# Kernel tuning notes

Measured on AMD Instinct MI355X. Metric: run time of the kernel, lower is better.

## Reference

```python
import jax, jax.numpy as jnp
import numpy as np

NBITS = 3      # weight LSQ bits
PBITS = 8      # partial-sum LSQ bits
EPS = 1e-5


def round_ste(x):
    # straight-through round: identity gradient
    return x + jax.lax.stop_gradient(jnp.round(x) - x)


def lsq(x, alpha, nbits):
    # learned-step-size quantize/dequantize (symmetric signed)
    qn = -(2 ** (nbits - 1))
    qp = 2 ** (nbits - 1) - 1
    return round_ste(jnp.clip(x / alpha, qn, qp)) * alpha


def split_views(x):
    # x: [B,C,H,W] -> 9 shifted views of the 1-padded input, stacked [9,B,C,H,W]
    B, C, H, W = x.shape
    xp = jnp.pad(x, ((0, 0), (0, 0), (1, 1), (1, 1)))
    views = [xp[:, :, di:di + H, dj:dj + W] for dj in range(3) for di in range(3)]
    return jnp.stack(views, 0)


def split_conv3x3(x, w, wa, pa):
    # 3x3 conv emulated as 9 shifted 1x1 LSQ convs with quantized partial-sum accumulate
    # w: [9,O,C] per-tap 1x1 weights, wa: [9] weight step sizes, pa: [9] psum step sizes
    xs = split_views(x)                                      # [9,B,C,H,W]
    wq = jax.vmap(lambda wk, ak: lsq(wk, ak, NBITS))(w, wa)  # [9,O,C]
    ps = jnp.einsum('kbchw,koc->kbohw', xs, wq)              # 9 partial sums
    psq = lsq(ps, pa[:, None, None, None, None], PBITS)      # PartialSumLSQ each tap
    return psq.sum(0)                                        # accumulate -> [B,O,H,W]


def batchnorm(x, g, b):
    m = x.mean((0, 2, 3), keepdims=True)
    v = x.var((0, 2, 3), keepdims=True)
    return (x - m) / jnp.sqrt(v + EPS) * g[None, :, None, None] + b[None, :, None, None]


def setup_inputs() -> dict:
    key = jax.random.key(0)
    ks = jax.random.split(key, 8)
    B, C, O, H, W = 16, 128, 128, 56, 56
    x = jax.random.normal(ks[0], (B, C, H, W), jnp.float32)
    w1 = jax.random.normal(ks[1], (9, O, C), jnp.float32) * 0.05
    w2 = jax.random.normal(ks[2], (9, O, O), jnp.float32) * 0.05
    qp_w = 2 ** (NBITS - 1) - 1
    wa1 = 2.0 * jnp.mean(jnp.abs(w1), axis=(1, 2)) / np.sqrt(qp_w)
    wa2 = 2.0 * jnp.mean(jnp.abs(w2), axis=(1, 2)) / np.sqrt(qp_w)
    pa1 = jnp.full((9,), 0.05, jnp.float32)
    pa2 = jnp.full((9,), 0.05, jnp.float32)
    g1 = jnp.ones((O,), jnp.float32); b1 = jnp.zeros((O,), jnp.float32)
    g2 = jnp.ones((O,), jnp.float32); b2 = jnp.zeros((O,), jnp.float32)
    return {'x': x, 'w1': w1, 'wa1': wa1, 'pa1': pa1, 'g1': g1, 'b1': b1,
            'w2': w2, 'wa2': wa2, 'pa2': pa2, 'g2': g2, 'b2': b2}


def reference(x, w1, wa1, pa1, g1, b1, w2, wa2, pa2, g2, b2):
    identity = x
    out = split_conv3x3(x, w1, wa1, pa1)
    out = jax.nn.relu(batchnorm(out, g1, b1))
    out = split_conv3x3(out, w2, wa2, pa2)
    out = batchnorm(out, g2, b2)
    return jax.nn.relu(out + identity)
```

## Files before the change

### kernel.cpp

```cpp
#include <hip/hip_runtime.h>
#include <math.h>

typedef _Float16 f16;
typedef _Float16 half8 __attribute__((ext_vector_type(8)));
typedef float floatx16 __attribute__((ext_vector_type(16)));
typedef unsigned int u32;

#define HW_     3136
#define NPC     50176.0f
#define PB      3364
#define PPLANE  53824
#define ASTRIDE (2 * PPLANE * 16)

#define SW(c, px) (((px) + ((c) >> 2) + ((c) & 3) * 8) & 63)

typedef __attribute__((address_space(3))) u32 lds_u32;
typedef __attribute__((address_space(1))) u32 glb_u32;
__device__ __forceinline__ void async_copy16(const void* g, void* l) {
    __builtin_amdgcn_global_load_lds((const glb_u32*)g, (lds_u32*)l, 16, 0, 0);
}

__global__ __launch_bounds__(256) void prelude_kernel(
        const float* __restrict__ x, char* __restrict__ X2,
        const float* __restrict__ w1, const float* __restrict__ wa1,
        const float* __restrict__ w2, const float* __restrict__ wa2,
        f16* __restrict__ W2a, f16* __restrict__ W2b,
        float* __restrict__ stats) {
    const int t = threadIdx.x;
    if (blockIdx.x < 784) {
        const int blk = blockIdx.x;
        if (blk == 0 && t < 512) stats[t] = 0.f;
        const int b = blk / 49;
        const int p0 = (blk - b * 49) * 64;
        const int px = t & 63;
        const int cq = t >> 6;
        const int p = p0 + px;
        const int h = p / 56;
        const int w = p - h * 56;
        const size_t pp = (size_t)b * PB + (h + 1) * 58 + (w + 1);
        const float* xb = x + (size_t)b * 128 * HW_ + p;
#pragma unroll
        for (int s = 0; s < 4; ++s) {
            const int cg = s * 4 + cq;
            half8 hv, lv;
#pragma unroll
            for (int j = 0; j < 8; ++j) {
                const float v = xb[(size_t)(cg * 8 + j) * HW_];
                const f16 hh = (f16)v;
                hv[j] = hh;
                lv[j] = (f16)(v - (float)hh);
            }
            *(half8*)(X2 + ((size_t)cg * PPLANE + pp) * 16) = hv;
            *(half8*)(X2 + ((size_t)(cg + 16) * PPLANE + pp) * 16) = lv;
        }
    } else if (blockIdx.x < 928) {
        const int idx = (blockIdx.x - 784) * 256 + t;
        const float* w;
        const float* wa;
        f16* o;
        int m;
        if (idx < 18432) { w = w1; wa = wa1; o = W2a; m = idx; }
        else             { w = w2; wa = wa2; o = W2b; m = idx - 18432; }
        const int tap = m >> 11;
        const int r = m & 2047;
        const int k2 = r >> 7;
        const int oc = r & 127;
        const float a = wa[tap];
        const float* src = w + ((size_t)(tap * 128 + oc) * 128 + k2 * 8);
        half8 hv;
#pragma unroll
        for (int j = 0; j < 8; ++j)
            hv[j] = (f16)rintf(fminf(fmaxf(src[j] / a, -4.f), 3.f));
        *(half8*)(o + (size_t)m * 8) = hv;
    } else {
        const int m = (blockIdx.x - 928) * 256 + t;
        const int k2 = m / 3648;
        const int r = m - k2 * 3648;
        const int b = r / 228;
        const int j = r - b * 228;
        int h, w;
        if (j < 58)        { h = 0;  w = j; }
        else if (j < 116)  { h = 57; w = j - 58; }
        else { const int k = j - 116; h = 1 + (k >> 1); w = (k & 1) * 57; }
        const size_t chunk = (size_t)k2 * PPLANE + (size_t)b * PB + h * 58 + w;
        float4 z = {0.f, 0.f, 0.f, 0.f};
        *(float4*)(X2 + chunk * 16) = z;
    }
}

__global__ __launch_bounds__(256, 2) void conv_kernel(
        const char* __restrict__ X2, const char* __restrict__ W2,
        const float* __restrict__ wav, const float* __restrict__ pav,
        float* __restrict__ cbuf, float* __restrict__ stats) {
    __shared__ f16 Bls[2][16384];
    __shared__ float red[512];
    const int t = threadIdx.x;
    const int lane = t & 63;
    const int wv = t >> 6;
    const int wm = wv & 1, wn = wv >> 1;
    const int tile = (blockIdx.x & 7) * 49 + (blockIdx.x >> 3);
    const int kh = lane >> 5;
    const int ln = lane & 31;

    int ppad[2];
#pragma unroll
    for (int mt = 0; mt < 2; ++mt) {
        const int gp = tile * 128 + wm * 64 + mt * 32 + ln;
        const int b = gp / HW_;
        const int p = gp - b * HW_;
        const int h = p / 56;
        const int w = p - h * 56;
        ppad[mt] = b * PB + (h + 1) * 58 + (w + 1);
    }
    int bdsoff[2];
#pragma unroll
    for (int nt = 0; nt < 2; ++nt)
        bdsoff[nt] = (kh * 128 + wn * 64 + nt * 32 + ln) * 16;
    const int sbase = wv * 8;

    floatx16 facc[2][2];
#pragma unroll
    for (int mt = 0; mt < 2; ++mt)
#pragma unroll
        for (int nt = 0; nt < 2; ++nt)
#pragma unroll
            for (int r = 0; r < 16; ++r) facc[mt][nt][r] = 0.f;

#pragma unroll
    for (int i = 0; i < 8; ++i)
        async_copy16(W2 + (((sbase + i) * 64 + lane) << 4),
                     (void*)&Bls[0][(sbase + i) * 512]);
    int aoff[2], aoffn[2];
#pragma unroll
    for (int mt = 0; mt < 2; ++mt) {
        aoff[mt] = ((ppad[mt] - 59) + kh * PPLANE) << 4;
        aoffn[mt] = aoff[mt];
    }
    half8 afr[2][8];
#pragma unroll
    for (int s0 = 0; s0 < 8; ++s0)
#pragma unroll
        for (int mt = 0; mt < 2; ++mt)
            afr[mt][s0] = *(const half8*)(X2 + aoff[mt] + s0 * ASTRIDE);
    __syncthreads();

    for (int tap = 0; tap < 9; ++tap) {
        const float pak = pav[tap];
        const float s1 = wav[tap] / pak;
        const char* bcur = (const char*)&Bls[tap & 1][0];
        if (tap < 8) {
            const char* wt = W2 + (tap + 1) * 32768;
            f16* bnxt = &Bls[(tap + 1) & 1][0];
#pragma unroll
            for (int i = 0; i < 8; ++i)
                async_copy16(wt + (((sbase + i) * 64 + lane) << 4),
                             (void*)&bnxt[(sbase + i) * 512]);
            const int dn = ((tap + 1) % 3 - 1) * 58 + ((tap + 1) / 3 - 1);
#pragma unroll
            for (int mt = 0; mt < 2; ++mt)
                aoffn[mt] = ((ppad[mt] + dn) + kh * PPLANE) << 4;
        }
        half8 bds[2][2];
#pragma unroll
        for (int nt = 0; nt < 2; ++nt)
#pragma unroll
            for (int sl = 0; sl < 2; ++sl)
                bds[nt][sl] = *(const half8*)(bcur + sl * 4096 + bdsoff[nt]);

        floatx16 acc[2][2];
#pragma unroll
        for (int mt = 0; mt < 2; ++mt)
#pragma unroll
            for (int nt = 0; nt < 2; ++nt)
#pragma unroll
                for (int r = 0; r < 16; ++r) acc[mt][nt][r] = 0.f;

#pragma unroll
        for (int s = 0; s < 16; ++s) {
#pragma unroll
            for (int nt = 0; nt < 2; ++nt)
#pragma unroll
                for (int mt = 0; mt < 2; ++mt)
                    acc[mt][nt] = __builtin_amdgcn_mfma_f32_32x32x16_f16(
                        afr[mt][s & 7], bds[nt][s & 1], acc[mt][nt], 0, 0, 0);
            if (s <= 13) {
                const int kf2 = (s + 2) & 7;
#pragma unroll
                for (int nt = 0; nt < 2; ++nt)
                    bds[nt][s & 1] =
                        *(const half8*)(bcur + kf2 * 4096 + bdsoff[nt]);
            }
            if (s < 8) {
#pragma unroll
                for (int mt = 0; mt < 2; ++mt)
                    afr[mt][s & 7] =
                        *(const half8*)(X2 + aoff[mt] + (s + 8) * ASTRIDE);
            } else if (tap < 8) {
#pragma unroll
                for (int mt = 0; mt < 2; ++mt)
                    afr[mt][s & 7] =
                        *(const half8*)(X2 + aoffn[mt] + (s - 8) * ASTRIDE);
            }
        }

#pragma unroll
        for (int mt = 0; mt < 2; ++mt)
#pragma unroll
            for (int nt = 0; nt < 2; ++nt)
#pragma unroll
                for (int r = 0; r < 16; ++r) {
                    const float q = rintf(__builtin_amdgcn_fmed3f(
                        acc[mt][nt][r] * s1, -128.f, 127.f));
                    facc[mt][nt][r] = fmaf(q, pak, facc[mt][nt][r]);
                }
        aoff[0] = aoffn[0];
        aoff[1] = aoffn[1];
        __syncthreads();
    }

    const int gpb = tile * 128 + wm * 64;
    const int ocb = wn * 64 + ln;
#pragma unroll
    for (int mt = 0; mt < 2; ++mt)
#pragma unroll
        for (int r = 0; r < 16; ++r) {
            const int row = (r & 3) + 8 * (r >> 2) + 4 * kh;
            const int gp = gpb + mt * 32 + row;
            float* rp = cbuf + (size_t)gp * 128 + ocb;
            rp[0]  = facc[mt][0][r];
            rp[32] = facc[mt][1][r];
        }

    float sv[2], qv[2];
#pragma unroll
    for (int nt = 0; nt < 2; ++nt) {
        float s = 0.f, q = 0.f;
#pragma unroll
        for (int mt = 0; mt < 2; ++mt)
#pragma unroll
            for (int r = 0; r < 16; ++r) {
                const float v = facc[mt][nt][r];
                s += v;
                q = fmaf(v, v, q);
            }
        s += __shfl_xor(s, 32, 64);
        q += __shfl_xor(q, 32, 64);
        sv[nt] = s; qv[nt] = q;
    }
    if (lane < 32) {
#pragma unroll
        for (int nt = 0; nt < 2; ++nt) {
            const int oc = wn * 64 + nt * 32 + lane;
            red[oc * 2 + wm] = sv[nt];
            red[256 + oc * 2 + wm] = qv[nt];
        }
    }
    __syncthreads();
    if (t < 128) {
        atomicAdd(&stats[t],       red[2 * t] + red[2 * t + 1]);
        atomicAdd(&stats[128 + t], red[256 + 2 * t] + red[256 + 2 * t + 1]);
    }
}

__global__ __launch_bounds__(256) void bn_split_kernel(
        const float* __restrict__ cbuf, const float* __restrict__ stats,
        const float* __restrict__ g, const float* __restrict__ bb,
        char* __restrict__ X2) {
    __shared__ float xs[8192];
    __shared__ float scs[128], shs[128];
    const int t = threadIdx.x;
    if (t < 128) {
        const float m = stats[t] * (1.f / NPC);
        const float var = stats[128 + t] * (1.f / NPC) - m * m;
        const float inv = 1.f / sqrtf(var + 1e-5f);
        const float sc = g[t] * inv;
        scs[t] = sc;
        shs[t] = bb[t] - m * sc;
    }
    __syncthreads();
    const int blk = blockIdx.x;
#pragma unroll
    for (int i = 0; i < 8; ++i) {
        const int idx = i * 256 + t;
        const int px = idx >> 5;
        const int q = idx & 31;
        const float4 v = *(const float4*)&cbuf[(size_t)(blk * 64 + px) * 128 + q * 4];
        const float vv[4] = {v.x, v.y, v.z, v.w};
#pragma unroll
        for (int j = 0; j < 4; ++j) {
            const int c = q * 4 + j;
            xs[c * 64 + SW(c, px)] = fmaxf(fmaf(vv[j], scs[c], shs[c]), 0.f);
        }
    }
    __syncthreads();
    const int b = blk / 49;
    const int p0 = (blk - b * 49) * 64;
    const int px = t & 63;
    const int cq = t >> 6;
    const int p = p0 + px;
    const int h = p / 56;
    const int w = p - h * 56;
    const size_t pp = (size_t)b * PB + (h + 1) * 58 + (w + 1);
#pragma unroll
    for (int s = 0; s < 4; ++s) {
        const int cg = s * 4 + cq;
        half8 hv, lv;
#pragma unroll
        for (int j = 0; j < 8; ++j) {
            const int c = cg * 8 + j;
            const float v = xs[c * 64 + SW(c, px)];
            const f16 hh = (f16)v;
            hv[j] = hh;
            lv[j] = (f16)(v - (float)hh);
        }
        *(half8*)(X2 + ((size_t)cg * PPLANE + pp) * 16) = hv;
        *(half8*)(X2 + ((size_t)(cg + 16) * PPLANE + pp) * 16) = lv;
    }
}

__global__ __launch_bounds__(256) void final_kernel(
        const float* __restrict__ cbuf, const float* __restrict__ stats,
        const float* __restrict__ g, const float* __restrict__ bb,
        const float* __restrict__ resid, float* __restrict__ out) {
    __shared__ float xs[8192];
    __shared__ float scs[128], shs[128];
    const int t = threadIdx.x;
    if (t < 128) {
        const float m = stats[t] * (1.f / NPC);
        const float var = stats[128 + t] * (1.f / NPC) - m * m;
        const float inv = 1.f / sqrtf(var + 1e-5f);
        const float sc = g[t] * inv;
        scs[t] = sc;
        shs[t] = bb[t] - m * sc;
    }
    __syncthreads();
    const int blk = blockIdx.x;
#pragma unroll
    for (int i = 0; i < 8; ++i) {
        const int idx = i * 256 + t;
        const int px = idx >> 5;
        const int q = idx & 31;
        const float4 v = *(const float4*)&cbuf[(size_t)(blk * 64 + px) * 128 + q * 4];
        const float vv[4] = {v.x, v.y, v.z, v.w};
#pragma unroll
        for (int j = 0; j < 4; ++j) {
            const int c = q * 4 + j;
            xs[c * 64 + SW(c, px)] = fmaf(vv[j], scs[c], shs[c]);
        }
    }
    __syncthreads();
    const int b = blk / 49;
    const int p0 = (blk - b * 49) * 64;
    const int lane = t & 63, wq = t >> 6;
#pragma unroll
    for (int i = 0; i < 32; ++i) {
        const int c = i * 4 + wq;
        const float v = xs[c * 64 + SW(c, lane)];
        const size_t gi = (size_t)(b * 128 + c) * HW_ + p0 + lane;
        out[gi] = fmaxf(v + resid[gi], 0.f);
    }
}

extern "C" void kernel_launch(void* const* d_in, const int* in_sizes, int n_in,
                              void* d_out, int out_size, void* d_ws, size_t ws_size,
                              hipStream_t stream) {
    const float* x   = (const float*)d_in[0];
    const float* w1  = (const float*)d_in[1];
    const float* wa1 = (const float*)d_in[2];
    const float* pa1 = (const float*)d_in[3];
    const float* g1  = (const float*)d_in[4];
    const float* b1  = (const float*)d_in[5];
    const float* w2  = (const float*)d_in[6];
    const float* wa2 = (const float*)d_in[7];
    const float* pa2 = (const float*)d_in[8];
    const float* g2  = (const float*)d_in[9];
    const float* b2  = (const float*)d_in[10];
    float* out = (float*)d_out;

    char* ws = (char*)d_ws;
    char*  X2    = ws;
    float* cbuf  = (float*)(ws + 27557888);
    f16*   W2a   = (f16*)(ws + 53248000);
    f16*   W2b   = (f16*)(ws + 53542912);
    float* stats = (float*)(ws + 53837824);
    float* stats1 = stats;
    float* stats2 = stats + 256;

    hipLaunchKernelGGL(prelude_kernel, dim3(1384), dim3(256), 0, stream,
                       x, X2, w1, wa1, w2, wa2, W2a, W2b, stats);
    hipLaunchKernelGGL(conv_kernel, dim3(392), dim3(256), 0, stream,
                       X2, (const char*)W2a, wa1, pa1, cbuf, stats1);
    hipLaunchKernelGGL(bn_split_kernel, dim3(784), dim3(256), 0, stream,
                       cbuf, stats1, g1, b1, X2);
    hipLaunchKernelGGL(conv_kernel, dim3(392), dim3(256), 0, stream,
                       X2, (const char*)W2b, wa2, pa2, cbuf, stats2);
    hipLaunchKernelGGL(final_kernel, dim3(784), dim3(256), 0, stream,
                       cbuf, stats2, g2, b2, x, out);
}
```

Baseline: 209.3 us.

## Fuse all five stages into one cooperative persistent kernel with grid syncs

Folds prelude, both convs, bn_split and final into a single cooperative kernel of 392 blocks. Stages are separated by grid.sync(), and each block processes several prelude, bnsplit and final units. This removes four kernel launch boundaries and their tail drains. In exchange, the memory-bound phases run at reduced parallelism (392 blocks doing serialized units), the grid barriers add cost, and the kernel falls back to separate launches if the cooperative launch fails.

```diff
diff --git a/kernel.cpp b/kernel.cpp
--- a/kernel.cpp
+++ b/kernel.cpp
@@ -1,5 +1,8 @@
 #include <hip/hip_runtime.h>
+#include <hip/hip_cooperative_groups.h>
 #include <math.h>
+
+namespace cg = cooperative_groups;
 
 typedef _Float16 f16;
 typedef _Float16 half8 __attribute__((ext_vector_type(8)));
@@ -20,15 +23,15 @@
     __builtin_amdgcn_global_load_lds((const glb_u32*)g, (lds_u32*)l, 16, 0, 0);
 }
 
-__global__ __launch_bounds__(256) void prelude_kernel(
-        const float* __restrict__ x, char* __restrict__ X2,
+__device__ __forceinline__ void prelude_unit(
+        int unit, const float* __restrict__ x, char* __restrict__ X2,
         const float* __restrict__ w1, const float* __restrict__ wa1,
         const float* __restrict__ w2, const float* __restrict__ wa2,
         f16* __restrict__ W2a, f16* __restrict__ W2b,
         float* __restrict__ stats) {
     const int t = threadIdx.x;
-    if (blockIdx.x < 784) {
-        const int blk = blockIdx.x;
+    if (unit < 784) {
+        const int blk = unit;
         if (blk == 0 && t < 512) stats[t] = 0.f;
         const int b = blk / 49;
         const int p0 = (blk - b * 49) * 64;
@@ -53,8 +56,8 @@
             *(half8*)(X2 + ((size_t)cg * PPLANE + pp) * 16) = hv;
             *(half8*)(X2 + ((size_t)(cg + 16) * PPLANE + pp) * 16) = lv;
         }
-    } else if (blockIdx.x < 928) {
-        const int idx = (blockIdx.x - 784) * 256 + t;
+    } else if (unit < 928) {
+        const int idx = (unit - 784) * 256 + t;
         const float* w;
         const float* wa;
         f16* o;
@@ -73,7 +76,7 @@
             hv[j] = (f16)rintf(fminf(fmaxf(src[j] / a, -4.f), 3.f));
         *(half8*)(o + (size_t)m * 8) = hv;
     } else {
-        const int m = (blockIdx.x - 928) * 256 + t;
+        const int m = (unit - 928) * 256 + t;
         const int k2 = m / 3648;
         const int r = m - k2 * 3648;
         const int b = r / 228;
@@ -88,12 +91,13 @@
     }
 }
 
-__global__ __launch_bounds__(256, 2) void conv_kernel(
+__device__ __forceinline__ void conv_phase(
         const char* __restrict__ X2, const char* __restrict__ W2,
         const float* __restrict__ wav, const float* __restrict__ pav,
-        float* __restrict__ cbuf, float* __restrict__ stats) {
-    __shared__ f16 Bls[2][16384];
-    __shared__ float red[512];
+        float* __restrict__ cbuf, float* __restrict__ stats,
+        char* smem) {
+    f16 (*Bls)[16384] = (f16 (*)[16384])smem;
+    float* red = (float*)(smem + 65536);
     const int t = threadIdx.x;
     const int lane = t & 63;
     const int wv = t >> 6;
@@ -262,12 +266,13 @@
     }
 }
 
-__global__ __launch_bounds__(256) void bn_split_kernel(
-        const float* __restrict__ cbuf, const float* __restrict__ stats,
+__device__ __forceinline__ void bnsplit_unit(
+        int blk, const float* __restrict__ cbuf, const float* __restrict__ stats,
         const float* __restrict__ g, const float* __restrict__ bb,
-        char* __restrict__ X2) {
-    __shared__ float xs[8192];
-    __shared__ float scs[128], shs[128];
+        char* __restrict__ X2, char* smem) {
+    float* xs = (float*)smem;
+    float* scs = (float*)(smem + 32768);
+    float* shs = (float*)(smem + 33280);
     const int t = threadIdx.x;
     if (t < 128) {
         const float m = stats[t] * (1.f / NPC);
@@ -278,7 +283,6 @@
         shs[t] = bb[t] - m * sc;
     }
     __syncthreads();
-    const int blk = blockIdx.x;
 #pragma unroll
     for (int i = 0; i < 8; ++i) {
         const int idx = i * 256 + t;
@@ -316,14 +320,16 @@
         *(half8*)(X2 + ((size_t)cg * PPLANE + pp) * 16) = hv;
         *(half8*)(X2 + ((size_t)(cg + 16) * PPLANE + pp) * 16) = lv;
     }
-}
-
-__global__ __launch_bounds__(256) void final_kernel(
-        const float* __restrict__ cbuf, const float* __restrict__ stats,
+    __syncthreads();
+}
+
+__device__ __forceinline__ void final_unit(
+        int blk, const float* __restrict__ cbuf, const float* __restrict__ stats,
         const float* __restrict__ g, const float* __restrict__ bb,
-        const float* __restrict__ resid, float* __restrict__ out) {
-    __shared__ float xs[8192];
-    __shared__ float scs[128], shs[128];
+        const float* __restrict__ resid, float* __restrict__ out, char* smem) {
+    float* xs = (float*)smem;
+    float* scs = (float*)(smem + 32768);
+    float* shs = (float*)(smem + 33280);
     const int t = threadIdx.x;
     if (t < 128) {
         const float m = stats[t] * (1.f / NPC);
@@ -334,7 +340,6 @@
         shs[t] = bb[t] - m * sc;
     }
     __syncthreads();
-    const int blk = blockIdx.x;
 #pragma unroll
     for (int i = 0; i < 8; ++i) {
         const int idx = i * 256 + t;
@@ -359,6 +364,76 @@
         const size_t gi = (size_t)(b * 128 + c) * HW_ + p0 + lane;
         out[gi] = fmaxf(v + resid[gi], 0.f);
     }
+    __syncthreads();
+}
+
+__global__ __launch_bounds__(256, 2) void mega_kernel(
+        const float* __restrict__ x,
+        const float* __restrict__ w1, const float* __restrict__ wa1,
+        const float* __restrict__ pa1, const float* __restrict__ g1,
+        const float* __restrict__ b1,
+        const float* __restrict__ w2, const float* __restrict__ wa2,
+        const float* __restrict__ pa2, const float* __restrict__ g2,
+        const float* __restrict__ b2, float* __restrict__ out,
+        char* __restrict__ X2, float* __restrict__ cbuf,
+        f16* __restrict__ W2a, f16* __restrict__ W2b,
+        float* __restrict__ stats) {
+    __shared__ __align__(16) char smem[67584];
+    cg::grid_group grid = cg::this_grid();
+
+#pragma unroll
+    for (int i = 0; i < 4; ++i) {
+        const int u = i * 392 + blockIdx.x;
+        if (u < 1384)
+            prelude_unit(u, x, X2, w1, wa1, w2, wa2, W2a, W2b, stats);
+    }
+    grid.sync();
+
+    conv_phase(X2, (const char*)W2a, wa1, pa1, cbuf, stats, smem);
+    grid.sync();
+
+    bnsplit_unit(2 * blockIdx.x,     cbuf, stats, g1, b1, X2, smem);
+    bnsplit_unit(2 * blockIdx.x + 1, cbuf, stats, g1, b1, X2, smem);
+    grid.sync();
+
+    conv_phase(X2, (const char*)W2b, wa2, pa2, cbuf, stats + 256, smem);
+    grid.sync();
+
+    final_unit(2 * blockIdx.x,     cbuf, stats + 256, g2, b2, x, out, smem);
+    final_unit(2 * blockIdx.x + 1, cbuf, stats + 256, g2, b2, x, out, smem);
+}
+
+__global__ __launch_bounds__(256) void prelude_kernel(
+        const float* __restrict__ x, char* __restrict__ X2,
+        const float* __restrict__ w1, const float* __restrict__ wa1,
+        const float* __restrict__ w2, const float* __restrict__ wa2,
+        f16* __restrict__ W2a, f16* __restrict__ W2b,
+        float* __restrict__ stats) {
+    prelude_unit(blockIdx.x, x, X2, w1, wa1, w2, wa2, W2a, W2b, stats);
+}
+
+__global__ __launch_bounds__(256, 2) void conv_kernel(
+        const char* __restrict__ X2, const char* __restrict__ W2,
+        const float* __restrict__ wav, const float* __restrict__ pav,
+        float* __restrict__ cbuf, float* __restrict__ stats) {
+    __shared__ __align__(16) char smem[67584];
+    conv_phase(X2, W2, wav, pav, cbuf, stats, smem);
+}
+
+__global__ __launch_bounds__(256) void bn_split_kernel(
+        const float* __restrict__ cbuf, const float* __restrict__ stats,
+        const float* __restrict__ g, const float* __restrict__ bb,
+        char* __restrict__ X2) {
+    __shared__ __align__(16) char smem[33792];
+    bnsplit_unit(blockIdx.x, cbuf, stats, g, bb, X2, smem);
+}
+
+__global__ __launch_bounds__(256) void final_kernel(
+        const float* __restrict__ cbuf, const float* __restrict__ stats,
+        const float* __restrict__ g, const float* __restrict__ bb,
+        const float* __restrict__ resid, float* __restrict__ out) {
+    __shared__ __align__(16) char smem[33792];
+    final_unit(blockIdx.x, cbuf, stats, g, bb, resid, out, smem);
 }
 
 extern "C" void kernel_launch(void* const* d_in, const int* in_sizes, int n_in,
@@ -383,17 +458,27 @@
     f16*   W2a   = (f16*)(ws + 53248000);
     f16*   W2b   = (f16*)(ws + 53542912);
     float* stats = (float*)(ws + 53837824);
-    float* stats1 = stats;
-    float* stats2 = stats + 256;
-
-    hipLaunchKernelGGL(prelude_kernel, dim3(1384), dim3(256), 0, stream,
-                       x, X2, w1, wa1, w2, wa2, W2a, W2b, stats);
-    hipLaunchKernelGGL(conv_kernel, dim3(392), dim3(256), 0, stream,
-                       X2, (const char*)W2a, wa1, pa1, cbuf, stats1);
-    hipLaunchKernelGGL(bn_split_kernel, dim3(784), dim3(256), 0, stream,
-                       cbuf, stats1, g1, b1, X2);
-    hipLaunchKernelGGL(conv_kernel, dim3(392), dim3(256), 0, stream,
-                       X2, (const char*)W2b, wa2, pa2, cbuf, stats2);
-    hipLaunchKernelGGL(final_kernel, dim3(784), dim3(256), 0, stream,
-                       cbuf, stats2, g2, b2, x, out);
-}
+
+    void* args[17] = {
+        (void*)&x, (void*)&w1, (void*)&wa1, (void*)&pa1, (void*)&g1,
+        (void*)&b1, (void*)&w2, (void*)&wa2, (void*)&pa2, (void*)&g2,
+        (void*)&b2, (void*)&out, (void*)&X2, (void*)&cbuf, (void*)&W2a,
+        (void*)&W2b, (void*)&stats
+    };
+    hipError_t err = hipLaunchCooperativeKernel(
+        (const void*)mega_kernel, dim3(392), dim3(256), args, 0, stream);
+    if (err != hipSuccess) {
+        float* stats1 = stats;
+        float* stats2 = stats + 256;
+        hipLaunchKernelGGL(prelude_kernel, dim3(1384), dim3(256), 0, stream,
+                           x, X2, w1, wa1, w2, wa2, W2a, W2b, stats);
+        hipLaunchKernelGGL(conv_kernel, dim3(392), dim3(256), 0, stream,
+                           X2, (const char*)W2a, wa1, pa1, cbuf, stats1);
+        hipLaunchKernelGGL(bn_split_kernel, dim3(784), dim3(256), 0, stream,
+                           cbuf, stats1, g1, b1, X2);
+        hipLaunchKernelGGL(conv_kernel, dim3(392), dim3(256), 0, stream,
+                           X2, (const char*)W2b, wa2, pa2, cbuf, stats2);
+        hipLaunchKernelGGL(final_kernel, dim3(784), dim3(256), 0, stream,
+                           cbuf, stats2, g2, b2, x, out);
+    }
+}
```

New measurement: 487.3 us. +132.8%, slower.

## Fuse BN epilogues into conv kernels via grid-wide atomic semaphore

Applied to the files above, without the earlier changes.

Merges each conv kernel with the following batchnorm kernel (bn_split or final). A global atomic counter acts as a grid barrier: each of the 392 blocks waits until all blocks have added their statistics, then applies BN to its own two 64-pixel tiles. This removes two kernel launches and their gaps. It relies on all 392 blocks being co-resident, which holds at 2 blocks per CU on a 256-CU part but would deadlock otherwise. It also writes X2 in place while other blocks may still be reading halo pixels for conv1.

```diff
diff --git a/kernel.cpp b/kernel.cpp
--- a/kernel.cpp
+++ b/kernel.cpp
@@ -25,11 +25,14 @@
         const float* __restrict__ w1, const float* __restrict__ wa1,
         const float* __restrict__ w2, const float* __restrict__ wa2,
         f16* __restrict__ W2a, f16* __restrict__ W2b,
-        float* __restrict__ stats) {
+        float* __restrict__ stats, u32* __restrict__ cnt) {
     const int t = threadIdx.x;
     if (blockIdx.x < 784) {
         const int blk = blockIdx.x;
-        if (blk == 0 && t < 512) stats[t] = 0.f;
+        if (blk == 0) {
+            if (t < 512) stats[t] = 0.f;
+            if (t == 0) { cnt[0] = 0u; cnt[1] = 0u; }
+        }
         const int b = blk / 49;
         const int p0 = (blk - b * 49) * 64;
         const int px = t & 63;
@@ -88,12 +91,13 @@
     }
 }
 
-__global__ __launch_bounds__(256, 2) void conv_kernel(
+__device__ __forceinline__ int conv_phase(
         const char* __restrict__ X2, const char* __restrict__ W2,
         const float* __restrict__ wav, const float* __restrict__ pav,
-        float* __restrict__ cbuf, float* __restrict__ stats) {
-    __shared__ f16 Bls[2][16384];
-    __shared__ float red[512];
+        float* __restrict__ cbuf, float* __restrict__ stats,
+        char* smem) {
+    f16 (*Bls)[16384] = (f16 (*)[16384])smem;
+    float* red = (float*)(smem + 65536);
     const int t = threadIdx.x;
     const int lane = t & 63;
     const int wv = t >> 6;
@@ -260,104 +264,147 @@
         atomicAdd(&stats[t],       red[2 * t] + red[2 * t + 1]);
         atomicAdd(&stats[128 + t], red[256 + 2 * t] + red[256 + 2 * t + 1]);
     }
-}
-
-__global__ __launch_bounds__(256) void bn_split_kernel(
-        const float* __restrict__ cbuf, const float* __restrict__ stats,
-        const float* __restrict__ g, const float* __restrict__ bb,
-        char* __restrict__ X2) {
-    __shared__ float xs[8192];
-    __shared__ float scs[128], shs[128];
+    return tile;
+}
+
+__device__ __forceinline__ void stats_semaphore(u32* cnt) {
+    asm volatile("s_waitcnt vmcnt(0)" ::: "memory");
+    __syncthreads();
+    if (threadIdx.x == 0) {
+        __hip_atomic_fetch_add(cnt, 1u, __ATOMIC_RELAXED,
+                               __HIP_MEMORY_SCOPE_AGENT);
+        while (__hip_atomic_load(cnt, __ATOMIC_RELAXED,
+                                 __HIP_MEMORY_SCOPE_AGENT) < 392u)
+            __builtin_amdgcn_s_sleep(8);
+    }
+    __syncthreads();
+}
+
+__device__ __forceinline__ void bn_coeffs(
+        const float* __restrict__ stats, const float* __restrict__ g,
+        const float* __restrict__ bb, float* scs, float* shs) {
     const int t = threadIdx.x;
     if (t < 128) {
-        const float m = stats[t] * (1.f / NPC);
-        const float var = stats[128 + t] * (1.f / NPC) - m * m;
+        const float s0 = __hip_atomic_load((float*)&stats[t],
+                __ATOMIC_RELAXED, __HIP_MEMORY_SCOPE_AGENT);
+        const float s1 = __hip_atomic_load((float*)&stats[128 + t],
+                __ATOMIC_RELAXED, __HIP_MEMORY_SCOPE_AGENT);
+        const float m = s0 * (1.f / NPC);
+        const float var = s1 * (1.f / NPC) - m * m;
         const float inv = 1.f / sqrtf(var + 1e-5f);
         const float sc = g[t] * inv;
         scs[t] = sc;
         shs[t] = bb[t] - m * sc;
     }
     __syncthreads();
-    const int blk = blockIdx.x;
-#pragma unroll
-    for (int i = 0; i < 8; ++i) {
-        const int idx = i * 256 + t;
-        const int px = idx >> 5;
-        const int q = idx & 31;
-        const float4 v = *(const float4*)&cbuf[(size_t)(blk * 64 + px) * 128 + q * 4];
-        const float vv[4] = {v.x, v.y, v.z, v.w};
-#pragma unroll
-        for (int j = 0; j < 4; ++j) {
-            const int c = q * 4 + j;
-            xs[c * 64 + SW(c, px)] = fmaxf(fmaf(vv[j], scs[c], shs[c]), 0.f);
-        }
-    }
-    __syncthreads();
-    const int b = blk / 49;
-    const int p0 = (blk - b * 49) * 64;
-    const int px = t & 63;
-    const int cq = t >> 6;
-    const int p = p0 + px;
-    const int h = p / 56;
-    const int w = p - h * 56;
-    const size_t pp = (size_t)b * PB + (h + 1) * 58 + (w + 1);
-#pragma unroll
-    for (int s = 0; s < 4; ++s) {
-        const int cg = s * 4 + cq;
-        half8 hv, lv;
-#pragma unroll
-        for (int j = 0; j < 8; ++j) {
-            const int c = cg * 8 + j;
-            const float v = xs[c * 64 + SW(c, px)];
-            const f16 hh = (f16)v;
-            hv[j] = hh;
-            lv[j] = (f16)(v - (float)hh);
-        }
-        *(half8*)(X2 + ((size_t)cg * PPLANE + pp) * 16) = hv;
-        *(half8*)(X2 + ((size_t)(cg + 16) * PPLANE + pp) * 16) = lv;
-    }
-}
-
-__global__ __launch_bounds__(256) void final_kernel(
-        const float* __restrict__ cbuf, const float* __restrict__ stats,
+}
+
+__global__ __launch_bounds__(256, 2) void conv_bn_kernel(
+        const char* __restrict__ X2, const char* __restrict__ W2,
+        const float* __restrict__ wav, const float* __restrict__ pav,
+        float* __restrict__ cbuf, float* __restrict__ stats,
         const float* __restrict__ g, const float* __restrict__ bb,
-        const float* __restrict__ resid, float* __restrict__ out) {
-    __shared__ float xs[8192];
-    __shared__ float scs[128], shs[128];
+        char* __restrict__ X2o, u32* __restrict__ cnt) {
+    __shared__ __align__(16) char smem[67584];
+    const int tile = conv_phase(X2, W2, wav, pav, cbuf, stats, smem);
+    stats_semaphore(cnt);
+
+    float* xs = (float*)smem;
+    float* scs = (float*)(smem + 32768);
+    float* shs = (float*)(smem + 33280);
+    bn_coeffs(stats, g, bb, scs, shs);
     const int t = threadIdx.x;
-    if (t < 128) {
-        const float m = stats[t] * (1.f / NPC);
-        const float var = stats[128 + t] * (1.f / NPC) - m * m;
-        const float inv = 1.f / sqrtf(var + 1e-5f);
-        const float sc = g[t] * inv;
-        scs[t] = sc;
-        shs[t] = bb[t] - m * sc;
-    }
-    __syncthreads();
-    const int blk = blockIdx.x;
-#pragma unroll
-    for (int i = 0; i < 8; ++i) {
-        const int idx = i * 256 + t;
-        const int px = idx >> 5;
-        const int q = idx & 31;
-        const float4 v = *(const float4*)&cbuf[(size_t)(blk * 64 + px) * 128 + q * 4];
-        const float vv[4] = {v.x, v.y, v.z, v.w};
-#pragma unroll
-        for (int j = 0; j < 4; ++j) {
-            const int c = q * 4 + j;
-            xs[c * 64 + SW(c, px)] = fmaf(vv[j], scs[c], shs[c]);
-        }
-    }
-    __syncthreads();
-    const int b = blk / 49;
-    const int p0 = (blk - b * 49) * 64;
-    const int lane = t & 63, wq = t >> 6;
-#pragma unroll
-    for (int i = 0; i < 32; ++i) {
-        const int c = i * 4 + wq;
-        const float v = xs[c * 64 + SW(c, lane)];
-        const size_t gi = (size_t)(b * 128 + c) * HW_ + p0 + lane;
-        out[gi] = fmaxf(v + resid[gi], 0.f);
+#pragma unroll
+    for (int u = 0; u < 2; ++u) {
+        const int blk = 2 * tile + u;
+#pragma unroll
+        for (int i = 0; i < 8; ++i) {
+            const int idx = i * 256 + t;
+            const int px = idx >> 5;
+            const int q = idx & 31;
+            const float4 v =
+                *(const float4*)&cbuf[(size_t)(blk * 64 + px) * 128 + q * 4];
+            const float vv[4] = {v.x, v.y, v.z, v.w};
+#pragma unroll
+            for (int j = 0; j < 4; ++j) {
+                const int c = q * 4 + j;
+                xs[c * 64 + SW(c, px)] =
+                    fmaxf(fmaf(vv[j], scs[c], shs[c]), 0.f);
+            }
+        }
+        __syncthreads();
+        const int b = blk / 49;
+        const int p0 = (blk - b * 49) * 64;
+        const int px = t & 63;
+        const int cq = t >> 6;
+        const int p = p0 + px;
+        const int h = p / 56;
+        const int w = p - h * 56;
+        const size_t pp = (size_t)b * PB + (h + 1) * 58 + (w + 1);
+#pragma unroll
+        for (int s = 0; s < 4; ++s) {
+            const int cg = s * 4 + cq;
+            half8 hv, lv;
+#pragma unroll
+            for (int j = 0; j < 8; ++j) {
+                const int c = cg * 8 + j;
+                const float v = xs[c * 64 + SW(c, px)];
+                const f16 hh = (f16)v;
+                hv[j] = hh;
+                lv[j] = (f16)(v - (float)hh);
+            }
+            *(half8*)(X2o + ((size_t)cg * PPLANE + pp) * 16) = hv;
+            *(half8*)(X2o + ((size_t)(cg + 16) * PPLANE + pp) * 16) = lv;
+        }
+        __syncthreads();
+    }
+}
+
+__global__ __launch_bounds__(256, 2) void conv_final_kernel(
+        const char* __restrict__ X2, const char* __restrict__ W2,
+        const float* __restrict__ wav, const float* __restrict__ pav,
+        float* __restrict__ cbuf, float* __restrict__ stats,
+        const float* __restrict__ g, const float* __restrict__ bb,
+        const float* __restrict__ resid, float* __restrict__ out,
+        u32* __restrict__ cnt) {
+    __shared__ __align__(16) char smem[67584];
+    const int tile = conv_phase(X2, W2, wav, pav, cbuf, stats, smem);
+    stats_semaphore(cnt);
+
+    float* xs = (float*)smem;
+    float* scs = (float*)(smem + 32768);
+    float* shs = (float*)(smem + 33280);
+    bn_coeffs(stats, g, bb, scs, shs);
+    const int t = threadIdx.x;
+#pragma unroll
+    for (int u = 0; u < 2; ++u) {
+        const int blk = 2 * tile + u;
+#pragma unroll
+        for (int i = 0; i < 8; ++i) {
+            const int idx = i * 256 + t;
+            const int px = idx >> 5;
+            const int q = idx & 31;
+            const float4 v =
+                *(const float4*)&cbuf[(size_t)(blk * 64 + px) * 128 + q * 4];
+            const float vv[4] = {v.x, v.y, v.z, v.w};
+#pragma unroll
+            for (int j = 0; j < 4; ++j) {
+                const int c = q * 4 + j;
+                xs[c * 64 + SW(c, px)] = fmaf(vv[j], scs[c], shs[c]);
+            }
+        }
+        __syncthreads();
+        const int b = blk / 49;
+        const int p0 = (blk - b * 49) * 64;
+        const int lane = t & 63, wq = t >> 6;
+#pragma unroll
+        for (int i = 0; i < 32; ++i) {
+            const int c = i * 4 + wq;
+            const float v = xs[c * 64 + SW(c, lane)];
+            const size_t gi = (size_t)(b * 128 + c) * HW_ + p0 + lane;
+            out[gi] = fmaxf(v + resid[gi], 0.f);
+        }
+        __syncthreads();
     }
 }
 
@@ -383,17 +430,16 @@
     f16*   W2a   = (f16*)(ws + 53248000);
     f16*   W2b   = (f16*)(ws + 53542912);
     float* stats = (float*)(ws + 53837824);
+    u32*   cnt   = (u32*)(ws + 53839872);
     float* stats1 = stats;
     float* stats2 = stats + 256;
 
     hipLaunchKernelGGL(prelude_kernel, dim3(1384), dim3(256), 0, stream,
-                       x, X2, w1, wa1, w2, wa2, W2a, W2b, stats);
-    hipLaunchKernelGGL(conv_kernel, dim3(392), dim3(256), 0, stream,
-                       X2, (const char*)W2a, wa1, pa1, cbuf, stats1);
-    hipLaunchKernelGGL(bn_split_kernel, dim3(784), dim3(256), 0, stream,
-                       cbuf, stats1, g1, b1, X2);
-    hipLaunchKernelGGL(conv_kernel, dim3(392), dim3(256), 0, stream,
-                       X2, (const char*)W2b, wa2, pa2, cbuf, stats2);
-    hipLaunchKernelGGL(final_kernel, dim3(784), dim3(256), 0, stream,
-                       cbuf, stats2, g2, b2, x, out);
-}
+                       x, X2, w1, wa1, w2, wa2, W2a, W2b, stats, cnt);
+    hipLaunchKernelGGL(conv_bn_kernel, dim3(392), dim3(256), 0, stream,
+                       X2, (const char*)W2a, wa1, pa1, cbuf, stats1,
+                       g1, b1, X2, cnt);
+    hipLaunchKernelGGL(conv_final_kernel, dim3(392), dim3(256), 0, stream,
+                       X2, (const char*)W2b, wa2, pa2, cbuf, stats2,
+                       g2, b2, x, out, cnt + 1);
+}
```

Result: slower. 266.1 us (+27.1%).
